# Kernel tuning notes

Hardware: AMD Instinct MI355X
Metric: run time of the kernel (lower is better)

Reference implementation:

```python
import jax, jax.numpy as jnp
import numpy as np

B, S, D, H = 2, 2048, 1024, 16
DK = D // H


def setup_inputs() -> dict:
    key = jax.random.key(0)
    ks = jax.random.split(key, 11)
    scale = 1.0 / np.sqrt(D)
    inp = {
        "q": jax.random.normal(ks[0], (B, S, D), jnp.float32),
        "k": jax.random.normal(ks[1], (B, S, D), jnp.float32),
        "v": jax.random.normal(ks[2], (B, S, D), jnp.float32),
        "mask": jnp.tril(jnp.ones((S, S), jnp.int32))[None, None],  # causal [1,1,S,S]
        "wq": jax.random.normal(ks[3], (D, D), jnp.float32) * scale,
        "bq": jnp.zeros((D,), jnp.float32),
        "wk": jax.random.normal(ks[4], (D, D), jnp.float32) * scale,
        "bk": jnp.zeros((D,), jnp.float32),
        "wv": jax.random.normal(ks[5], (D, D), jnp.float32) * scale,
        "bv": jnp.zeros((D,), jnp.float32),
        "wo": jax.random.normal(ks[6], (D, D), jnp.float32) * scale,
        "bo": jnp.zeros((D,), jnp.float32),
    }
    return inp


def _split_heads(x):  # [B,S,D] -> [B,H,S,DK]
    return x.reshape(B, S, H, DK).transpose(0, 2, 1, 3)


def reference(q, k, v, mask, wq, bq, wk, bk, wv, bv, wo, bo):
    # projections (nn.Linear: x @ W.T + b)
    query = _split_heads(q @ wq.T + bq)
    key_ = _split_heads(k @ wk.T + bk)
    value = _split_heads(v @ wv.T + bv)
    # scaled dot-product attention, full [B,H,S,S] scores as in source
    scores = jnp.einsum('bhqd,bhkd->bhqk', query, key_) / np.sqrt(DK)
    scores = jnp.where(mask == 0, jnp.float32(-1e9), scores)
    attn = jax.nn.softmax(scores, axis=-1)
    out = jnp.einsum('bhqk,bhkd->bhqd', attn, value)
    out = out.transpose(0, 2, 1, 3).reshape(B, S, D)
    x = out @ wo.T + bo
    return x, attn
```

## Files before the change

### kernel.cpp

```cpp
#include <hip/hip_runtime.h>
#include <hip/hip_bf16.h>

typedef __attribute__((ext_vector_type(8))) __bf16 bf16x8;
typedef __attribute__((ext_vector_type(4))) __bf16 bf16x4;
typedef __attribute__((ext_vector_type(4))) float f32x4;

#define MFMA16(a, b, c) __builtin_amdgcn_mfma_f32_16x16x32_bf16((a), (b), (c), 0, 0, 0)

#define SEQ 2048
#define DIM 1024

__global__ __launch_bounds__(256) void cvt_bf16(
    const float* __restrict__ q, const float* __restrict__ k, const float* __restrict__ v,
    const float* __restrict__ wq, const float* __restrict__ wk, const float* __restrict__ wv,
    const float* __restrict__ wo,
    __bf16* __restrict__ qb, __bf16* __restrict__ kb, __bf16* __restrict__ vb,
    __bf16* __restrict__ wqb, __bf16* __restrict__ wkb, __bf16* __restrict__ wvb,
    __bf16* __restrict__ wob) {
  int a = blockIdx.y;
  const float* src = (a == 0) ? q : (a == 1) ? k : (a == 2) ? v
                    : (a == 3) ? wq : (a == 4) ? wk : (a == 5) ? wv : wo;
  __bf16* dst = (a == 0) ? qb : (a == 1) ? kb : (a == 2) ? vb
               : (a == 3) ? wqb : (a == 4) ? wkb : (a == 5) ? wvb : wob;
  size_t n = (a < 3) ? (size_t)(2 * SEQ * DIM) : (size_t)(DIM * DIM);
  size_t i = ((size_t)blockIdx.x * 256 + threadIdx.x) * 8;
  if (i >= n) return;
  float4 f0 = *(const float4*)&src[i];
  float4 f1 = *(const float4*)&src[i + 4];
  bf16x8 o = {(__bf16)f0.x, (__bf16)f0.y, (__bf16)f0.z, (__bf16)f0.w,
              (__bf16)f1.x, (__bf16)f1.y, (__bf16)f1.z, (__bf16)f1.w};
  *(bf16x8*)&dst[i] = o;
}

__global__ __launch_bounds__(256) void qkv_gemm(
    const __bf16* __restrict__ qI, const __bf16* __restrict__ kI, const __bf16* __restrict__ vI,
    const __bf16* __restrict__ wqI, const __bf16* __restrict__ wkI, const __bf16* __restrict__ wvI,
    const float* __restrict__ bqI, const float* __restrict__ bkI, const float* __restrict__ bvI,
    __bf16* __restrict__ Qp, __bf16* __restrict__ Kp, __bf16* __restrict__ Vt) {
  const int N = 1024, K = 1024;
  int z = blockIdx.z;
  const __bf16* A = (z == 0) ? qI : (z == 1) ? kI : vI;
  const __bf16* W = (z == 0) ? wqI : (z == 1) ? wkI : wvI;
  const float* bias = (z == 0) ? bqI : (z == 1) ? bkI : bvI;

  __shared__ __bf16 As[128][40];
  __shared__ __bf16 Bs[128][40];

  int tid = threadIdx.x;
  int wave = tid >> 6, lane = tid & 63;
  int quad = lane >> 4, l16 = lane & 15;
  int wm = (wave >> 1) * 64, wn = (wave & 1) * 64;
  int m0 = blockIdx.y * 128, n0 = blockIdx.x * 128;
  int sr = tid >> 3;
  int sc = (tid & 7) * 4;

  f32x4 acc[4][4] = {};

  bf16x4 pa[4], pw[4];
#pragma unroll
  for (int i = 0; i < 4; i++) {
    int r = sr + i * 32;
    pa[i] = *(const bf16x4*)&A[(size_t)(m0 + r) * K + sc];
    pw[i] = *(const bf16x4*)&W[(size_t)(n0 + r) * K + sc];
  }

  for (int k0 = 0; k0 < K; k0 += 32) {
    __syncthreads();
#pragma unroll
    for (int i = 0; i < 4; i++) {
      int r = sr + i * 32;
      *(bf16x4*)&As[r][sc] = pa[i];
      *(bf16x4*)&Bs[r][sc] = pw[i];
    }
    __syncthreads();
    if (k0 + 32 < K) {
#pragma unroll
      for (int i = 0; i < 4; i++) {
        int r = sr + i * 32;
        pa[i] = *(const bf16x4*)&A[(size_t)(m0 + r) * K + k0 + 32 + sc];
        pw[i] = *(const bf16x4*)&W[(size_t)(n0 + r) * K + k0 + 32 + sc];
      }
    }
    bf16x8 af[4], bfv[4];
#pragma unroll
    for (int i = 0; i < 4; i++) af[i] = *(bf16x8*)&As[wm + i * 16 + l16][quad * 8];
#pragma unroll
    for (int j = 0; j < 4; j++) bfv[j] = *(bf16x8*)&Bs[wn + j * 16 + l16][quad * 8];
#pragma unroll
    for (int i = 0; i < 4; i++)
#pragma unroll
      for (int j = 0; j < 4; j++) acc[i][j] = MFMA16(af[i], bfv[j], acc[i][j]);
  }

#pragma unroll
  for (int j = 0; j < 4; j++) {
    int col = n0 + wn + j * 16 + l16;
    float bj = bias[col];
    if (z == 2) {
#pragma unroll
      for (int i = 0; i < 4; i++) {
        int row0 = m0 + wm + i * 16 + quad * 4;
        int bb = row0 >> 11, s = row0 & 2047;
        bf16x4 pv = {(__bf16)(acc[i][j][0] + bj), (__bf16)(acc[i][j][1] + bj),
                     (__bf16)(acc[i][j][2] + bj), (__bf16)(acc[i][j][3] + bj)};
        *(bf16x4*)&Vt[((size_t)bb * 1024 + col) * SEQ + s] = pv;
      }
    } else {
      __bf16* C = (z == 0) ? Qp : Kp;
      float scale = (z == 0) ? 0.125f : 1.0f;
#pragma unroll
      for (int i = 0; i < 4; i++)
#pragma unroll
        for (int r = 0; r < 4; r++) {
          int row = m0 + wm + i * 16 + quad * 4 + r;
          C[(size_t)row * N + col] = (__bf16)((acc[i][j][r] + bj) * scale);
        }
    }
  }
}

__global__ __launch_bounds__(256) void out_gemm(
    const __bf16* __restrict__ A, const __bf16* __restrict__ W,
    const float* __restrict__ bias, float* __restrict__ C) {
  const int N = 1024, K = 1024;
  __shared__ __bf16 As[128][40];
  __shared__ __bf16 Bs[128][40];

  int tid = threadIdx.x;
  int wave = tid >> 6, lane = tid & 63;
  int quad = lane >> 4, l16 = lane & 15;
  int wm = (wave >> 1) * 64, wn = (wave & 1) * 64;
  int m0 = blockIdx.y * 128, n0 = blockIdx.x * 128;
  int sr = tid >> 3;
  int sc = (tid & 7) * 4;

  f32x4 acc[4][4] = {};

  bf16x4 pa[4], pw[4];
#pragma unroll
  for (int i = 0; i < 4; i++) {
    int r = sr + i * 32;
    pa[i] = *(const bf16x4*)&A[(size_t)(m0 + r) * K + sc];
    pw[i] = *(const bf16x4*)&W[(size_t)(n0 + r) * K + sc];
  }

  for (int k0 = 0; k0 < K; k0 += 32) {
    __syncthreads();
#pragma unroll
    for (int i = 0; i < 4; i++) {
      int r = sr + i * 32;
      *(bf16x4*)&As[r][sc] = pa[i];
      *(bf16x4*)&Bs[r][sc] = pw[i];
    }
    __syncthreads();
    if (k0 + 32 < K) {
#pragma unroll
      for (int i = 0; i < 4; i++) {
        int r = sr + i * 32;
        pa[i] = *(const bf16x4*)&A[(size_t)(m0 + r) * K + k0 + 32 + sc];
        pw[i] = *(const bf16x4*)&W[(size_t)(n0 + r) * K + k0 + 32 + sc];
      }
    }
    bf16x8 af[4], bfv[4];
#pragma unroll
    for (int i = 0; i < 4; i++) af[i] = *(bf16x8*)&As[wm + i * 16 + l16][quad * 8];
#pragma unroll
    for (int j = 0; j < 4; j++) bfv[j] = *(bf16x8*)&Bs[wn + j * 16 + l16][quad * 8];
#pragma unroll
    for (int i = 0; i < 4; i++)
#pragma unroll
      for (int j = 0; j < 4; j++) acc[i][j] = MFMA16(af[i], bfv[j], acc[i][j]);
  }

#pragma unroll
  for (int j = 0; j < 4; j++) {
    int col = n0 + wn + j * 16 + l16;
    float bj = bias[col];
#pragma unroll
    for (int i = 0; i < 4; i++)
#pragma unroll
      for (int r = 0; r < 4; r++) {
        int row = m0 + wm + i * 16 + quad * 4 + r;
        C[(size_t)row * N + col] = acc[i][j][r] + bj;
      }
  }
}

__global__ __launch_bounds__(256) void attn_fused(
    const __bf16* __restrict__ Qp, const __bf16* __restrict__ Kp,
    const __bf16* __restrict__ Vt, float* __restrict__ attn,
    __bf16* __restrict__ Oc) {
  int bh = blockIdx.y;
  int b = bh >> 4;
  int hofs = (bh & 15) * 64;
  int q0 = blockIdx.x * 64;

  int tid = threadIdx.x;
  int wave = tid >> 6, lane = tid & 63;
  int quad = lane >> 4, l16 = lane & 15;

  __shared__ __bf16 Qs[64][72];
  __shared__ __bf16 Ks[128][72];
  __shared__ __bf16 Vts[64][136];
  __shared__ __bf16 Ps[64][136];

  const size_t rowbase = (size_t)b * SEQ;
  const size_t vtbase = (size_t)bh * 64 * SEQ;

#pragma unroll
  for (int it = 0; it < 2; it++) {
    int flat = tid * 8 + it * 2048;
    int r = flat >> 6, c = flat & 63;
    *(bf16x8*)&Qs[r][c] = *(const bf16x8*)&Qp[(rowbase + q0 + r) * DIM + hofs + c];
  }
  __syncthreads();

  int qg = q0 + wave * 16 + l16;
  bf16x8 qfrag0 = *(bf16x8*)&Qs[wave * 16 + l16][quad * 8];
  bf16x8 qfrag1 = *(bf16x8*)&Qs[wave * 16 + l16][32 + quad * 8];

  float m_i = -1e30f, l_i = 0.f;
  int ktmax = (q0 + 63) >> 7;

  for (int kt = 0; kt <= ktmax; kt++) {
    int k0 = kt << 7;
    __syncthreads();
#pragma unroll
    for (int it = 0; it < 4; it++) {
      int flat = tid * 8 + it * 2048;
      int r = flat >> 6, c = flat & 63;
      *(bf16x8*)&Ks[r][c] = *(const bf16x8*)&Kp[(rowbase + k0 + r) * DIM + hofs + c];
    }
    __syncthreads();

    f32x4 sacc[8] = {};
#pragma unroll
    for (int t = 0; t < 8; t++) {
      bf16x8 a0 = *(bf16x8*)&Ks[t * 16 + l16][quad * 8];
      bf16x8 a1 = *(bf16x8*)&Ks[t * 16 + l16][32 + quad * 8];
      sacc[t] = MFMA16(a0, qfrag0, sacc[t]);
      sacc[t] = MFMA16(a1, qfrag1, sacc[t]);
    }

    bool diag = (kt == ktmax);
    float sv[32];
    float mx = -1e30f;
#pragma unroll
    for (int t = 0; t < 8; t++)
#pragma unroll
      for (int r = 0; r < 4; r++) {
        float s = sacc[t][r];
        int k = k0 + t * 16 + quad * 4 + r;
        if (diag && k > qg) s = -1e30f;
        sv[t * 4 + r] = s;
        mx = fmaxf(mx, s);
      }
    mx = fmaxf(mx, __shfl_xor(mx, 16));
    mx = fmaxf(mx, __shfl_xor(mx, 32));
    float mn = fmaxf(m_i, mx);
    float sum = 0.f;
#pragma unroll
    for (int i = 0; i < 32; i++) sum += __expf(sv[i] - mn);
    sum += __shfl_xor(sum, 16);
    sum += __shfl_xor(sum, 32);
    l_i = l_i * __expf(m_i - mn) + sum;
    m_i = mn;
  }

  float rl = 1.f / l_i;
  f32x4 oacc[4] = {};
  float* attn_bh = attn + (size_t)bh * SEQ * SEQ;
  float* attn_row = attn_bh + (size_t)qg * SEQ;

  for (int kt = 0; kt < SEQ / 128; kt++) {
    int k0 = kt << 7;
    if (kt <= ktmax) {
      __syncthreads();
#pragma unroll
      for (int it = 0; it < 4; it++) {
        int flat = tid * 8 + it * 2048;
        int r = flat >> 6, c = flat & 63;
        *(bf16x8*)&Ks[r][c] = *(const bf16x8*)&Kp[(rowbase + k0 + r) * DIM + hofs + c];
        int d = flat >> 7, c2 = flat & 127;
        *(bf16x8*)&Vts[d][c2] = *(const bf16x8*)&Vt[vtbase + (size_t)d * SEQ + k0 + c2];
      }
      __syncthreads();

      f32x4 sacc[8] = {};
#pragma unroll
      for (int t = 0; t < 8; t++) {
        bf16x8 a0 = *(bf16x8*)&Ks[t * 16 + l16][quad * 8];
        bf16x8 a1 = *(bf16x8*)&Ks[t * 16 + l16][32 + quad * 8];
        sacc[t] = MFMA16(a0, qfrag0, sacc[t]);
        sacc[t] = MFMA16(a1, qfrag1, sacc[t]);
      }

      bool diag = (kt == ktmax);
#pragma unroll
      for (int t = 0; t < 8; t++) {
        float p[4];
#pragma unroll
        for (int r = 0; r < 4; r++) {
          int k = k0 + t * 16 + quad * 4 + r;
          float s = sacc[t][r];
          p[r] = (!diag || k <= qg) ? __expf(s - m_i) * rl : 0.f;
        }
        *(float4*)&attn_row[k0 + t * 16 + quad * 4] = make_float4(p[0], p[1], p[2], p[3]);
        bf16x4 ph = {(__bf16)p[0], (__bf16)p[1], (__bf16)p[2], (__bf16)p[3]};
        *(bf16x4*)&Ps[wave * 16 + l16][t * 16 + quad * 4] = ph;
      }
      __syncthreads();

#pragma unroll
      for (int ks = 0; ks < 4; ks++) {
        bf16x8 a = *(bf16x8*)&Ps[wave * 16 + l16][ks * 32 + quad * 8];
#pragma unroll
        for (int dt = 0; dt < 4; dt++) {
          bf16x8 bb = *(bf16x8*)&Vts[dt * 16 + l16][ks * 32 + quad * 8];
          oacc[dt] = MFMA16(a, bb, oacc[dt]);
        }
      }
    } else {
      float4 z4 = make_float4(0.f, 0.f, 0.f, 0.f);
#pragma unroll
      for (int i = 0; i < 8; i++) {
        int f4 = tid + i * 256;
        int r = f4 >> 5;
        int c = (f4 & 31) * 4;
        *(float4*)&attn_bh[(size_t)(q0 + r) * SEQ + k0 + c] = z4;
      }
    }
  }

#pragma unroll
  for (int dt = 0; dt < 4; dt++)
#pragma unroll
    for (int rr = 0; rr < 4; rr++) {
      int row = q0 + wave * 16 + quad * 4 + rr;
      Oc[(rowbase + row) * DIM + hofs + dt * 16 + l16] = (__bf16)oacc[dt][rr];
    }
}

extern "C" void kernel_launch(void* const* d_in, const int* in_sizes, int n_in,
                              void* d_out, int out_size, void* d_ws, size_t ws_size,
                              hipStream_t stream) {
  const float* q = (const float*)d_in[0];
  const float* k = (const float*)d_in[1];
  const float* v = (const float*)d_in[2];
  const float* wq = (const float*)d_in[4];
  const float* bq = (const float*)d_in[5];
  const float* wk = (const float*)d_in[6];
  const float* bk = (const float*)d_in[7];
  const float* wv = (const float*)d_in[8];
  const float* bv = (const float*)d_in[9];
  const float* wo = (const float*)d_in[10];
  const float* bo = (const float*)d_in[11];

  float* xout = (float*)d_out;
  float* attn = xout + (size_t)2 * SEQ * DIM;

  const size_t NBS = (size_t)2 * SEQ * DIM;
  const size_t NW = (size_t)DIM * DIM;

  __bf16* Qp = (__bf16*)d_ws;
  __bf16* Kp = Qp + NBS;
  __bf16* Vt = Kp + NBS;
  __bf16* Oc = Vt + NBS;
  __bf16* qb = Oc + NBS;
  __bf16* kb = qb + NBS;
  __bf16* vb = kb + NBS;
  __bf16* wqb = vb + NBS;
  __bf16* wkb = wqb + NW;
  __bf16* wvb = wkb + NW;
  __bf16* wob = wvb + NW;

  dim3 blk(256);

  dim3 g0(2048, 7);
  cvt_bf16<<<g0, blk, 0, stream>>>(q, k, v, wq, wk, wv, wo,
                                   qb, kb, vb, wqb, wkb, wvb, wob);

  dim3 g1(8, 32, 3);
  qkv_gemm<<<g1, blk, 0, stream>>>(qb, kb, vb, wqb, wkb, wvb, bq, bk, bv, Qp, Kp, Vt);

  dim3 g2(32, 32);
  attn_fused<<<g2, blk, 0, stream>>>(Qp, Kp, Vt, attn, Oc);

  dim3 g3(8, 32);
  out_gemm<<<g3, blk, 0, stream>>>(Oc, wob, bo, xout);
}
```

Before: 778.7 us.

## Double-buffer GEMM tiles via direct global-to-LDS loads; load Q fragments directly

Both projection GEMMs now stage A and W tiles into double-buffered LDS using global_load_lds, which copies global memory straight into LDS without going through registers. This removes one barrier per k-step and the register round trip. The attention kernel drops its Q shared-memory staging and loads each lane's Q fragments directly from global memory. The LDS tiles lose their padding, so the MFMA fragment reads may hit more bank conflicts. Correctness also depends on the single barrier being enough to order the asynchronous LDS writes against reads of the buffer currently in use.

```diff
diff --git a/kernel.cpp b/kernel.cpp
--- a/kernel.cpp
+++ b/kernel.cpp
@@ -9,6 +9,12 @@
 
 #define SEQ 2048
 #define DIM 1024
+
+__device__ __forceinline__ void gload_lds16(const __bf16* g, __bf16* l) {
+  __builtin_amdgcn_global_load_lds(
+      (const __attribute__((address_space(1))) void*)g,
+      (__attribute__((address_space(3))) void*)l, 16, 0, 0);
+}
 
 __global__ __launch_bounds__(256) void cvt_bf16(
     const float* __restrict__ q, const float* __restrict__ k, const float* __restrict__ v,
@@ -43,53 +49,52 @@
   const __bf16* W = (z == 0) ? wqI : (z == 1) ? wkI : wvI;
   const float* bias = (z == 0) ? bqI : (z == 1) ? bkI : bvI;
 
-  __shared__ __bf16 As[128][40];
-  __shared__ __bf16 Bs[128][40];
+  __shared__ __bf16 As[2][128 * 32];
+  __shared__ __bf16 Bs[2][128 * 32];
 
   int tid = threadIdx.x;
   int wave = tid >> 6, lane = tid & 63;
   int quad = lane >> 4, l16 = lane & 15;
   int wm = (wave >> 1) * 64, wn = (wave & 1) * 64;
   int m0 = blockIdx.y * 128, n0 = blockIdx.x * 128;
-  int sr = tid >> 3;
-  int sc = (tid & 7) * 4;
+
+  int srow = wave * 16 + (lane >> 2);
+  int scol = (lane & 3) * 8;
+  const __bf16* Ab = &A[(size_t)(m0 + srow) * K + scol];
+  const __bf16* Wb = &W[(size_t)(n0 + srow) * K + scol];
+  int lo = wave * 512;
 
   f32x4 acc[4][4] = {};
 
-  bf16x4 pa[4], pw[4];
-#pragma unroll
-  for (int i = 0; i < 4; i++) {
-    int r = sr + i * 32;
-    pa[i] = *(const bf16x4*)&A[(size_t)(m0 + r) * K + sc];
-    pw[i] = *(const bf16x4*)&W[(size_t)(n0 + r) * K + sc];
-  }
-
+  {
+    gload_lds16(Ab, &As[0][lo]);
+    gload_lds16(Ab + (size_t)64 * K, &As[0][lo + 2048]);
+    gload_lds16(Wb, &Bs[0][lo]);
+    gload_lds16(Wb + (size_t)64 * K, &Bs[0][lo + 2048]);
+  }
+
+  int buf = 0;
   for (int k0 = 0; k0 < K; k0 += 32) {
     __syncthreads();
-#pragma unroll
-    for (int i = 0; i < 4; i++) {
-      int r = sr + i * 32;
-      *(bf16x4*)&As[r][sc] = pa[i];
-      *(bf16x4*)&Bs[r][sc] = pw[i];
-    }
-    __syncthreads();
     if (k0 + 32 < K) {
-#pragma unroll
-      for (int i = 0; i < 4; i++) {
-        int r = sr + i * 32;
-        pa[i] = *(const bf16x4*)&A[(size_t)(m0 + r) * K + k0 + 32 + sc];
-        pw[i] = *(const bf16x4*)&W[(size_t)(n0 + r) * K + k0 + 32 + sc];
-      }
-    }
+      int nb = buf ^ 1;
+      gload_lds16(Ab + k0 + 32, &As[nb][lo]);
+      gload_lds16(Ab + (size_t)64 * K + k0 + 32, &As[nb][lo + 2048]);
+      gload_lds16(Wb + k0 + 32, &Bs[nb][lo]);
+      gload_lds16(Wb + (size_t)64 * K + k0 + 32, &Bs[nb][lo + 2048]);
+    }
+    const __bf16* as = &As[buf][0];
+    const __bf16* bs = &Bs[buf][0];
     bf16x8 af[4], bfv[4];
 #pragma unroll
-    for (int i = 0; i < 4; i++) af[i] = *(bf16x8*)&As[wm + i * 16 + l16][quad * 8];
-#pragma unroll
-    for (int j = 0; j < 4; j++) bfv[j] = *(bf16x8*)&Bs[wn + j * 16 + l16][quad * 8];
+    for (int i = 0; i < 4; i++) af[i] = *(const bf16x8*)&as[(wm + i * 16 + l16) * 32 + quad * 8];
+#pragma unroll
+    for (int j = 0; j < 4; j++) bfv[j] = *(const bf16x8*)&bs[(wn + j * 16 + l16) * 32 + quad * 8];
 #pragma unroll
     for (int i = 0; i < 4; i++)
 #pragma unroll
       for (int j = 0; j < 4; j++) acc[i][j] = MFMA16(af[i], bfv[j], acc[i][j]);
+    buf ^= 1;
   }
 
 #pragma unroll
@@ -123,53 +128,52 @@
     const __bf16* __restrict__ A, const __bf16* __restrict__ W,
     const float* __restrict__ bias, float* __restrict__ C) {
   const int N = 1024, K = 1024;
-  __shared__ __bf16 As[128][40];
-  __shared__ __bf16 Bs[128][40];
+  __shared__ __bf16 As[2][128 * 32];
+  __shared__ __bf16 Bs[2][128 * 32];
 
   int tid = threadIdx.x;
   int wave = tid >> 6, lane = tid & 63;
   int quad = lane >> 4, l16 = lane & 15;
   int wm = (wave >> 1) * 64, wn = (wave & 1) * 64;
   int m0 = blockIdx.y * 128, n0 = blockIdx.x * 128;
-  int sr = tid >> 3;
-  int sc = (tid & 7) * 4;
+
+  int srow = wave * 16 + (lane >> 2);
+  int scol = (lane & 3) * 8;
+  const __bf16* Ab = &A[(size_t)(m0 + srow) * K + scol];
+  const __bf16* Wb = &W[(size_t)(n0 + srow) * K + scol];
+  int lo = wave * 512;
 
   f32x4 acc[4][4] = {};
 
-  bf16x4 pa[4], pw[4];
-#pragma unroll
-  for (int i = 0; i < 4; i++) {
-    int r = sr + i * 32;
-    pa[i] = *(const bf16x4*)&A[(size_t)(m0 + r) * K + sc];
-    pw[i] = *(const bf16x4*)&W[(size_t)(n0 + r) * K + sc];
-  }
-
+  {
+    gload_lds16(Ab, &As[0][lo]);
+    gload_lds16(Ab + (size_t)64 * K, &As[0][lo + 2048]);
+    gload_lds16(Wb, &Bs[0][lo]);
+    gload_lds16(Wb + (size_t)64 * K, &Bs[0][lo + 2048]);
+  }
+
+  int buf = 0;
   for (int k0 = 0; k0 < K; k0 += 32) {
     __syncthreads();
-#pragma unroll
-    for (int i = 0; i < 4; i++) {
-      int r = sr + i * 32;
-      *(bf16x4*)&As[r][sc] = pa[i];
-      *(bf16x4*)&Bs[r][sc] = pw[i];
-    }
-    __syncthreads();
     if (k0 + 32 < K) {
-#pragma unroll
-      for (int i = 0; i < 4; i++) {
-        int r = sr + i * 32;
-        pa[i] = *(const bf16x4*)&A[(size_t)(m0 + r) * K + k0 + 32 + sc];
-        pw[i] = *(const bf16x4*)&W[(size_t)(n0 + r) * K + k0 + 32 + sc];
-      }
-    }
+      int nb = buf ^ 1;
+      gload_lds16(Ab + k0 + 32, &As[nb][lo]);
+      gload_lds16(Ab + (size_t)64 * K + k0 + 32, &As[nb][lo + 2048]);
+      gload_lds16(Wb + k0 + 32, &Bs[nb][lo]);
+      gload_lds16(Wb + (size_t)64 * K + k0 + 32, &Bs[nb][lo + 2048]);
+    }
+    const __bf16* as = &As[buf][0];
+    const __bf16* bs = &Bs[buf][0];
     bf16x8 af[4], bfv[4];
 #pragma unroll
-    for (int i = 0; i < 4; i++) af[i] = *(bf16x8*)&As[wm + i * 16 + l16][quad * 8];
-#pragma unroll
-    for (int j = 0; j < 4; j++) bfv[j] = *(bf16x8*)&Bs[wn + j * 16 + l16][quad * 8];
+    for (int i = 0; i < 4; i++) af[i] = *(const bf16x8*)&as[(wm + i * 16 + l16) * 32 + quad * 8];
+#pragma unroll
+    for (int j = 0; j < 4; j++) bfv[j] = *(const bf16x8*)&bs[(wn + j * 16 + l16) * 32 + quad * 8];
 #pragma unroll
     for (int i = 0; i < 4; i++)
 #pragma unroll
       for (int j = 0; j < 4; j++) acc[i][j] = MFMA16(af[i], bfv[j], acc[i][j]);
+    buf ^= 1;
   }
 
 #pragma unroll
@@ -199,7 +203,6 @@
   int wave = tid >> 6, lane = tid & 63;
   int quad = lane >> 4, l16 = lane & 15;
 
-  __shared__ __bf16 Qs[64][72];
   __shared__ __bf16 Ks[128][72];
   __shared__ __bf16 Vts[64][136];
   __shared__ __bf16 Ps[64][136];
@@ -207,17 +210,11 @@
   const size_t rowbase = (size_t)b * SEQ;
   const size_t vtbase = (size_t)bh * 64 * SEQ;
 
-#pragma unroll
-  for (int it = 0; it < 2; it++) {
-    int flat = tid * 8 + it * 2048;
-    int r = flat >> 6, c = flat & 63;
-    *(bf16x8*)&Qs[r][c] = *(const bf16x8*)&Qp[(rowbase + q0 + r) * DIM + hofs + c];
-  }
-  __syncthreads();
-
   int qg = q0 + wave * 16 + l16;
-  bf16x8 qfrag0 = *(bf16x8*)&Qs[wave * 16 + l16][quad * 8];
-  bf16x8 qfrag1 = *(bf16x8*)&Qs[wave * 16 + l16][32 + quad * 8];
+
+  const __bf16* qpp = &Qp[(rowbase + qg) * DIM + hofs + quad * 8];
+  bf16x8 qfrag0 = *(const bf16x8*)qpp;
+  bf16x8 qfrag1 = *(const bf16x8*)(qpp + 32);
 
   float m_i = -1e30f, l_i = 0.f;
   int ktmax = (q0 + 63) >> 7;
```

After: 762.9 us (median of 2 runs). 2.0% less time.
